# Kernel optimization log

Measured on AMD Instinct MI355X. Metric: run time of the kernel, lower is better.

## Reference

```python
import jax, jax.numpy as jnp
import numpy as np

B, T_D, T_P = 64, 256, 1024
DRUG_DIM, PROT_DIM, D = 128, 128, 128
MAX_LEN = 1024
NEG = -1e9


def _linear_params(k, out_d, in_d):
    k1, k2 = jax.random.split(k)
    lim = 1.0 / np.sqrt(in_d)
    W = jax.random.uniform(k1, (out_d, in_d), minval=-lim, maxval=lim, dtype=jnp.float32)
    b = jax.random.uniform(k2, (out_d,), minval=-lim, maxval=lim, dtype=jnp.float32)
    return W, b


def setup_inputs() -> dict:
    key = jax.random.key(0)
    ks = jax.random.split(key, 13)
    inp = {
        'smiles_embeddings': jax.random.normal(ks[0], (B, T_D, DRUG_DIM), dtype=jnp.float32),
        'protein_embeddings': jax.random.normal(ks[1], (B, T_P, PROT_DIM), dtype=jnp.float32),
        'smiles_mask': jax.random.randint(ks[2], (B, T_D), 0, 2, dtype=jnp.int32),
        'protein_mask': jax.random.randint(ks[3], (B, T_P), 0, 2, dtype=jnp.int32),
        # torch inits pos_bias to zeros; small random values make the test nontrivial
        'pos_bias': 0.02 * jax.random.normal(ks[4], (MAX_LEN, MAX_LEN), dtype=jnp.float32),
    }
    names = [('Wqd', 'bqd', DRUG_DIM), ('Wkp', 'bkp', PROT_DIM), ('Wvp', 'bvp', PROT_DIM),
             ('Wqp', 'bqp', PROT_DIM), ('Wkd', 'bkd', DRUG_DIM), ('Wvd', 'bvd', DRUG_DIM),
             ('Wpd', 'bpd', D), ('Wpp', 'bpp', D)]
    for i, (wn, bn, in_d) in enumerate(names):
        W, b = _linear_params(ks[5 + i], D, in_d)
        inp[wn] = W
        inp[bn] = b
    return inp


def _lin(x, W, b):
    return x @ W.T + b


def _aft(q, k, v, pb_masked, Wp, bp):
    # q: [B,Ti,D]; k,v: [B,Tj,D]; pb_masked: [B,Ti,Tj]
    max_k = k.max(axis=1, keepdims=True)              # per (b,d) over seq j
    max_pb = pb_masked.max(axis=2, keepdims=True)     # per (b,i) over j
    exp_k = jnp.exp(k - max_k)                        # [B,Tj,D]
    exp_pb = jnp.exp(pb_masked - max_pb)              # [B,Ti,Tj]
    num = jnp.einsum('bij,bjd->bid', exp_pb, exp_k * v)
    den = jnp.einsum('bij,bjd->bid', exp_pb, exp_k)
    y = jax.nn.sigmoid(q) * num / den
    return _lin(y, Wp, bp)


def reference(smiles_embeddings, protein_embeddings, smiles_mask, protein_mask, pos_bias,
              Wqd, bqd, Wkp, bkp, Wvp, bvp, Wqp, bqp, Wkd, bkd, Wvd, bvd, Wpd, bpd, Wpp, bpp):
    Td = smiles_embeddings.shape[1]
    Tp = protein_embeddings.shape[1]
    combined = smiles_mask[:, :, None] * protein_mask[:, None, :]  # [B,Td,Tp]
    pb = pos_bias[:Td, :Tp][None]                                   # [1,Td,Tp]

    # drug queries attend over protein keys/values
    pb_d = jnp.where(combined == 0, NEG, pb)
    y_d = _aft(_lin(smiles_embeddings, Wqd, bqd),
               _lin(protein_embeddings, Wkp, bkp),
               _lin(protein_embeddings, Wvp, bvp), pb_d, Wpd, bpd)

    # protein queries attend over drug keys/values (transposed pos bias)
    pb_p = jnp.where(jnp.swapaxes(combined, 1, 2) == 0, NEG, jnp.swapaxes(pb, 1, 2))
    y_p = _aft(_lin(protein_embeddings, Wqp, bqp),
               _lin(smiles_embeddings, Wkd, bkd),
               _lin(smiles_embeddings, Wvd, bvd), pb_p, Wpp, bpp)

    y_d = jnp.where(smiles_mask[:, :, None] == 0, NEG, y_d).max(axis=1)   # [B,D]
    y_p = jnp.where(protein_mask[:, :, None] == 0, NEG, y_p).max(axis=1)  # [B,D]
    return y_d, y_p
```

## Files before the change

### kernel.cpp

```cpp
#include <hip/hip_runtime.h>
#include <cstdint>
#include <cstddef>

#define NEGV -1e9f

typedef __bf16 bf16x8 __attribute__((ext_vector_type(8)));
typedef float f32x4 __attribute__((ext_vector_type(4)));
typedef unsigned short us4 __attribute__((ext_vector_type(4)));
typedef unsigned short us8 __attribute__((ext_vector_type(8)));

__device__ __forceinline__ unsigned short f2bf(float f) {
  unsigned int u = __float_as_uint(f);
  u += 0x7fffu + ((u >> 16) & 1u);
  return (unsigned short)(u >> 16);
}
__device__ __forceinline__ float bf2f(unsigned short u) {
  return __uint_as_float(((unsigned)u) << 16);
}


__global__ void prep_kernel(const float* __restrict__ w0, const float* __restrict__ w1,
                            const float* __restrict__ w2, const float* __restrict__ w3,
                            const float* __restrict__ w4, const float* __restrict__ w5,
                            const float* __restrict__ w6, const float* __restrict__ w7,
                            unsigned short* __restrict__ Wbf,
                            const float* __restrict__ pb,
                            unsigned short* __restrict__ epb,
                            unsigned short* __restrict__ epbT,
                            unsigned int* __restrict__ outEnc) {
  __shared__ unsigned short t[32][33];
  const int blk = blockIdx.x, tid = threadIdx.x;
  if (blk < 64) {
    outEnc[blk * 256 + tid] = 0u;
    return;
  }
  if (blk < 192) {
    const float* Ws[8] = {w0, w1, w2, w3, w4, w5, w6, w7};
    int idx = (blk - 64) * 256 + tid;
    int mat = idx >> 12, off = idx & 4095;
    float4 v = *(const float4*)&Ws[mat][(size_t)off * 4];
    us4 p;
    p.x = f2bf(v.x); p.y = f2bf(v.y); p.z = f2bf(v.z); p.w = f2bf(v.w);
    *(us4*)&Wbf[(size_t)mat * 16384 + (size_t)off * 4] = p;
    return;
  }
  const int bid = blk - 192;
  const int j0 = (bid & 31) * 32, i0 = (bid >> 5) * 32;
  const int tx = tid & 31, ty = tid >> 5;
#pragma unroll
  for (int r = 0; r < 4; ++r) {
    int i = i0 + ty + r * 8;
    unsigned short u = f2bf(__expf(pb[(size_t)i * 1024 + j0 + tx]));
    epb[(size_t)i * 1024 + j0 + tx] = u;
    t[ty + r * 8][tx] = u;
  }
  __syncthreads();
#pragma unroll
  for (int r = 0; r < 4; ++r)
    epbT[(size_t)(j0 + ty + r * 8) * 256 + i0 + tx] = t[tx][ty + r * 8];
}

__global__ __launch_bounds__(256) void proj3_all(
    const float* __restrict__ smiles, const float* __restrict__ prot,
    const int* __restrict__ smask, const int* __restrict__ pmask,
    const unsigned short* __restrict__ Wbf,
    const float* __restrict__ bqd, const float* __restrict__ bkd, const float* __restrict__ bvd,
    const float* __restrict__ bqp, const float* __restrict__ bkp, const float* __restrict__ bvp,
    const unsigned short* __restrict__ epb, const unsigned short* __restrict__ epbT,
    unsigned short* __restrict__ AFd, unsigned short* __restrict__ AFp,
    unsigned short* __restrict__ SQd, unsigned short* __restrict__ BKd,
    unsigned short* __restrict__ BVd,
    unsigned short* __restrict__ SQp, unsigned short* __restrict__ BKp,
    unsigned short* __restrict__ BVp) {
  const int tid = threadIdx.x;

  if (blockIdx.x >= 1280) {
    int sid = (blockIdx.x - 1280) * 256 + tid;
    if (sid < 32768) {
      int lane = sid & 63, kt = (sid >> 6) & 31, it = sid >> 11;
      int i = it * 16 + (lane & 15), j = kt * 32 + (lane >> 4) * 8;
      *(us8*)&AFd[(size_t)sid * 8] = *(const us8*)&epb[(size_t)i * 1024 + j];
    } else {
      int s2 = sid - 32768;
      int lane = s2 & 63, kt = (s2 >> 6) & 7, it = s2 >> 9;
      int i = it * 16 + (lane & 15), j = kt * 32 + (lane >> 4) * 8;
      *(us8*)&AFp[(size_t)s2 * 8] = *(const us8*)&epbT[(size_t)i * 256 + j];
    }
    return;
  }

  __shared__ unsigned short xL[64 * 136];

  const float* X; const int* mask;
  const unsigned short *Wq, *Wk, *Wv;
  const float *bq, *bk_, *bv;
  unsigned short *SQ, *BK, *BV;
  int T, g0;
  if (blockIdx.x < 256) {
    X = smiles; mask = smask; T = 256; g0 = blockIdx.x * 64;
    Wq = Wbf; Wk = Wbf + 16384; Wv = Wbf + 32768;
    bq = bqd; bk_ = bkd; bv = bvd;
    SQ = SQd; BK = BKd; BV = BVd;
  } else {
    X = prot; mask = pmask; T = 1024; g0 = (blockIdx.x - 256) * 64;
    Wq = Wbf + 3 * 16384; Wk = Wbf + 4 * 16384; Wv = Wbf + 5 * 16384;
    bq = bqp; bk_ = bkp; bv = bvp;
    SQ = SQp; BK = BKp; BV = BVp;
  }
  const int b = g0 / T;
  const int tl0 = g0 - b * T;
  const int NIT = T / 16, NKT = T / 32;

#pragma unroll
  for (int r = 0; r < 8; ++r) {
    int i4 = tid + 256 * r;
    int t = i4 >> 5, k4 = (i4 & 31) * 4;
    float4 v = *(const float4*)&X[(size_t)(g0 + t) * 128 + k4];
    us4 p;
    p.x = f2bf(v.x); p.y = f2bf(v.y); p.z = f2bf(v.z); p.w = f2bf(v.w);
    *(us4*)&xL[t * 136 + k4] = p;
  }
  __syncthreads();

  const int lane = tid & 63, wave = tid >> 6;
  const int lo = lane & 15, hi = lane >> 4;
  const int d0 = wave * 32;

  f32x4 aQ[4][2], aK[4][2], aV[4][2];
#pragma unroll
  for (int a = 0; a < 4; ++a)
#pragma unroll
    for (int s = 0; s < 2; ++s)
#pragma unroll
      for (int r = 0; r < 4; ++r) { aQ[a][s][r] = 0.f; aK[a][s][r] = 0.f; aV[a][s][r] = 0.f; }

#pragma unroll
  for (int kt = 0; kt < 128; kt += 32) {
    bf16x8 bQ[2], bK[2], bV[2];
#pragma unroll
    for (int s = 0; s < 2; ++s) {
      size_t roff = (size_t)(d0 + s * 16 + lo) * 128 + kt + hi * 8;
      bQ[s] = *(const bf16x8*)&Wq[roff];
      bK[s] = *(const bf16x8*)&Wk[roff];
      bV[s] = *(const bf16x8*)&Wv[roff];
    }
#pragma unroll
    for (int a = 0; a < 4; ++a) {
      bf16x8 af = *(const bf16x8*)&xL[(a * 16 + lo) * 136 + kt + hi * 8];
#pragma unroll
      for (int s = 0; s < 2; ++s) {
        aQ[a][s] = __builtin_amdgcn_mfma_f32_16x16x32_bf16(af, bQ[s], aQ[a][s], 0, 0, 0);
        aK[a][s] = __builtin_amdgcn_mfma_f32_16x16x32_bf16(af, bK[s], aK[a][s], 0, 0, 0);
        aV[a][s] = __builtin_amdgcn_mfma_f32_16x16x32_bf16(af, bV[s], aV[a][s], 0, 0, 0);
      }
    }
  }

#pragma unroll
  for (int s = 0; s < 2; ++s) {
    int dt = (d0 >> 4) + s;
    float bb = bq[d0 + s * 16 + lo];
#pragma unroll
    for (int a = 0; a < 4; ++a) {
      int it = (tl0 >> 4) + a;
      us4 v;
#pragma unroll
      for (int r = 0; r < 4; ++r) {
        float q = aQ[a][s][r] + bb;
        v[r] = f2bf(1.f / (1.f + __expf(-q)));
      }
      ((us4*)SQ)[(((size_t)b * NIT + it) * 8 + dt) * 64 + lane] = v;
    }
  }

#pragma unroll
  for (int s = 0; s < 2; ++s) {
    int dt = (d0 >> 4) + s;
    float bbk = bk_[d0 + s * 16 + lo], bbv = bv[d0 + s * 16 + lo];
#pragma unroll
    for (int a = 0; a < 4; ++a) {
      int kt = (tl0 >> 5) + (a >> 1);
      int lane_f = ((a & 1) * 2 + (hi >> 1)) * 16 + lo;
      us4 vk, vv;
#pragma unroll
      for (int r = 0; r < 4; ++r) {
        int tg = g0 + a * 16 + hi * 4 + r;
        int mk = mask[tg];
        float ek = mk ? __expf(aK[a][s][r] + bbk) : 0.f;
        float ekv = ek * (aV[a][s][r] + bbv);
        vk[r] = f2bf(ek);
        vv[r] = f2bf(ekv);
      }
      size_t q4 = ((((size_t)b * NKT + kt) * 8 + dt) * 64 + lane_f) * 2 + (hi & 1);
      ((us4*)BK)[q4] = vk;
      ((us4*)BV)[q4] = vv;
    }
  }
}

__global__ __launch_bounds__(256, 3) void aft_all(
    const unsigned short* __restrict__ AFd, const unsigned short* __restrict__ AFp,
    const unsigned short* __restrict__ SQd, const unsigned short* __restrict__ BKd,
    const unsigned short* __restrict__ BVd,
    const unsigned short* __restrict__ SQp, const unsigned short* __restrict__ BKp,
    const unsigned short* __restrict__ BVp,
    const int* __restrict__ smask, const int* __restrict__ pmask,
    const unsigned short* __restrict__ Wbf,
    const float* __restrict__ bpd, const float* __restrict__ bpp,
    unsigned int* __restrict__ outEnc) {
  __shared__ unsigned short smem[8192 + 64 * 136];
  unsigned short* denL = smem;
  unsigned short* yL = smem + 8192;

  const int blk = blockIdx.x;
  const unsigned short *AF, *BK, *BV, *SQ, *Wp;
  const float* bp;
  const int* msk;
  unsigned int* oEnc;
  int b, i0, NKT, NIT;
  if (blk < 256) {
    b = blk & 63; i0 = (blk >> 6) * 64; NKT = 32; NIT = 16;
    AF = AFd; BK = BKp; BV = BVp; SQ = SQd;
    Wp = Wbf + 6 * 16384; bp = bpd; msk = smask + b * 256 + i0; oEnc = outEnc;
  } else {
    int k = blk - 256;
    b = k & 63; i0 = (k >> 6) * 64; NKT = 8; NIT = 64;
    AF = AFp; BK = BKd; BV = BVd; SQ = SQp;
    Wp = Wbf + 7 * 16384; bp = bpp; msk = pmask + b * 1024 + i0; oEnc = outEnc + 8192;
  }

  const int tid = threadIdx.x, lane = tid & 63, w = tid >> 6;
  const int lo = lane & 15, hi = lane >> 4;
  const int h = w & 1;
  const int isden = w >> 1;
  const int it0 = i0 >> 4;
  const int dt0 = h * 4;

  const unsigned short* Bb = (isden ? BK : BV) + (size_t)b * NKT * 8 * 64 * 8;

  f32x4 acc[4][4];
#pragma unroll
  for (int a = 0; a < 4; ++a)
#pragma unroll
    for (int n = 0; n < 4; ++n)
#pragma unroll
      for (int r = 0; r < 4; ++r) acc[a][n][r] = 0.f;

  bf16x8 af[4], bb[4];
#pragma unroll
  for (int a = 0; a < 4; ++a)
    af[a] = *(const bf16x8*)&AF[(((size_t)(it0 + a) * NKT + 0) * 64 + lane) * 8];
#pragma unroll
  for (int n = 0; n < 4; ++n)
    bb[n] = *(const bf16x8*)&Bb[(((size_t)0 * 8 + dt0 + n) * 64 + lane) * 8];

  for (int kt = 0; kt < NKT; ++kt) {
    const int k2 = (kt + 1 < NKT) ? kt + 1 : kt;
    bf16x8 afn[4], bbn[4];
#pragma unroll
    for (int a = 0; a < 4; ++a)
      afn[a] = *(const bf16x8*)&AF[(((size_t)(it0 + a) * NKT + k2) * 64 + lane) * 8];
#pragma unroll
    for (int n = 0; n < 4; ++n)
      bbn[n] = *(const bf16x8*)&Bb[(((size_t)k2 * 8 + dt0 + n) * 64 + lane) * 8];
#pragma unroll
    for (int a = 0; a < 4; ++a)
#pragma unroll
      for (int n = 0; n < 4; ++n)
        acc[a][n] = __builtin_amdgcn_mfma_f32_16x16x32_bf16(af[a], bb[n], acc[a][n], 0, 0, 0);
#pragma unroll
    for (int a = 0; a < 4; ++a) af[a] = afn[a];
#pragma unroll
    for (int n = 0; n < 4; ++n) bb[n] = bbn[n];
  }

  if (isden) {
#pragma unroll
    for (int a = 0; a < 4; ++a)
#pragma unroll
      for (int n = 0; n < 4; ++n) {
        us4 v;
#pragma unroll
        for (int r = 0; r < 4; ++r) v[r] = f2bf(acc[a][n][r]);
        ((us4*)denL)[((h * 4 + a) * 4 + n) * 64 + lane] = v;
      }
  }
  __syncthreads();

  if (!isden) {
#pragma unroll
    for (int a = 0; a < 4; ++a)
#pragma unroll
      for (int n = 0; n < 4; ++n) {
        us4 dv = ((const us4*)denL)[((h * 4 + a) * 4 + n) * 64 + lane];
        us4 q = ((const us4*)SQ)[(((size_t)b * NIT + it0 + a) * 8 + dt0 + n) * 64 + lane];
        int iL = a * 16 + hi * 4;
        int d = h * 64 + n * 16 + lo;
#pragma unroll
        for (int r = 0; r < 4; ++r) {
          float y = bf2f(q[r]) * __fdividef(acc[a][n][r], bf2f(dv[r]));
          yL[(iL + r) * 136 + d] = f2bf(y);
        }
      }
  }
  __syncthreads();

  const int wi2 = w * 16;
  f32x4 aZ[8];
#pragma unroll
  for (int n = 0; n < 8; ++n)
#pragma unroll
    for (int r = 0; r < 4; ++r) aZ[n][r] = 0.f;

#pragma unroll
  for (int kt = 0; kt < 128; kt += 32) {
    bf16x8 af2 = *(const bf16x8*)&yL[(wi2 + lo) * 136 + kt + hi * 8];
#pragma unroll
    for (int n = 0; n < 8; ++n) {
      bf16x8 bw = *(const bf16x8*)&Wp[(size_t)(n * 16 + lo) * 128 + kt + hi * 8];
      aZ[n] = __builtin_amdgcn_mfma_f32_16x16x32_bf16(af2, bw, aZ[n], 0, 0, 0);
    }
  }

#pragma unroll
  for (int n = 0; n < 8; ++n) {
    int d = n * 16 + lo;
    float bbia = bp[d];
    float m = NEGV;
#pragma unroll
    for (int r = 0; r < 4; ++r) {
      int iL = wi2 + hi * 4 + r;
      float z = aZ[n][r] + bbia;
      m = msk[iL] ? fmaxf(m, z) : m;
    }
    m = fmaxf(m, __shfl_xor(m, 16, 64));
    m = fmaxf(m, __shfl_xor(m, 32, 64));
    if (hi == 0) {
      unsigned bits = __float_as_uint(m);
      unsigned key = (bits & 0x80000000u) ? ~bits : (bits | 0x80000000u);
      atomicMax(&oEnc[b * 128 + d], key);
    }
  }
}

__global__ void out_decode(unsigned int* o) {
  int i = blockIdx.x * 256 + threadIdx.x;
  unsigned k = o[i];
  unsigned bits = (k & 0x80000000u) ? (k ^ 0x80000000u) : ~k;
  ((float*)o)[i] = __uint_as_float(bits);
}

extern "C" void kernel_launch(void* const* d_in, const int* in_sizes, int n_in,
                              void* d_out, int out_size, void* d_ws, size_t ws_size,
                              hipStream_t stream) {
  const float* smiles = (const float*)d_in[0];
  const float* prot   = (const float*)d_in[1];
  const int* smask = (const int*)d_in[2];
  const int* pmask = (const int*)d_in[3];
  const float* pos_bias = (const float*)d_in[4];
  const float* Wqd = (const float*)d_in[5];  const float* bqd = (const float*)d_in[6];
  const float* Wkp = (const float*)d_in[7];  const float* bkp = (const float*)d_in[8];
  const float* Wvp = (const float*)d_in[9];  const float* bvp = (const float*)d_in[10];
  const float* Wqp = (const float*)d_in[11]; const float* bqp = (const float*)d_in[12];
  const float* Wkd = (const float*)d_in[13]; const float* bkd = (const float*)d_in[14];
  const float* Wvd = (const float*)d_in[15]; const float* bvd = (const float*)d_in[16];
  const float* Wpd = (const float*)d_in[17]; const float* bpd = (const float*)d_in[18];
  const float* Wpp = (const float*)d_in[19]; const float* bpp = (const float*)d_in[20];

  unsigned short* u = (unsigned short*)d_ws;
  unsigned short* BKp_  = u;
  unsigned short* BVp_  = BKp_ + 8388608;
  unsigned short* BKd_  = BVp_ + 8388608;
  unsigned short* BVd_  = BKd_ + 2097152;
  unsigned short* SQd_  = BVd_ + 2097152;
  unsigned short* SQp_  = SQd_ + 2097152;
  unsigned short* epb_  = SQp_ + 8388608;
  unsigned short* epbT_ = epb_ + 262144;
  unsigned short* AFd_  = epbT_ + 262144;
  unsigned short* AFp_  = AFd_ + 262144;
  unsigned short* Wbf   = AFp_ + 262144;

  prep_kernel<<<448, 256, 0, stream>>>(Wqd, Wkd, Wvd, Wqp, Wkp, Wvp, Wpd, Wpp,
                                       Wbf, pos_bias, epb_, epbT_,
                                       (unsigned int*)d_out);

  proj3_all<<<1536, 256, 0, stream>>>(smiles, prot, smask, pmask, Wbf,
                                      bqd, bkd, bvd, bqp, bkp, bvp,
                                      epb_, epbT_, AFd_, AFp_,
                                      SQd_, BKd_, BVd_, SQp_, BKp_, BVp_);

  aft_all<<<1280, 256, 0, stream>>>(AFd_, AFp_, SQd_, BKd_, BVd_,
                                    SQp_, BKp_, BVp_, smask, pmask, Wbf,
                                    bpd, bpp, (unsigned int*)d_out);

  out_decode<<<64, 256, 0, stream>>>((unsigned int*)d_out);
}
```

Baseline: 190.5 us.

## Stage AFT GEMM operands in LDS via direct global-to-LDS loads with larger tiles

The AFT kernel goes from 256-thread blocks covering 64 query rows to 512-thread blocks covering 128 rows. Each k-step, the operand tiles for the exp-bias matrix and the exp(k)·v and exp(k) values are loaded cooperatively into shared memory with global_load_lds. Waves then read them from LDS, so each tile is fetched from global memory once and shared by several waves instead of being loaded per wave into registers. In exchange, the register double-buffered prefetch is gone and there are two block barriers per k-step, which may expose load latency. The tail of the kernel (the projection stage past the shown code) is not visible, so it is unclear whether it was adapted to 128 rows and 8 waves.

```diff
diff --git a/kernel.cpp b/kernel.cpp
--- a/kernel.cpp
+++ b/kernel.cpp
@@ -16,6 +16,12 @@
 }
 __device__ __forceinline__ float bf2f(unsigned short u) {
   return __uint_as_float(((unsigned)u) << 16);
+}
+
+__device__ __forceinline__ void gld16(const void* g, void* l) {
+  __builtin_amdgcn_global_load_lds(
+      (const __attribute__((address_space(1))) unsigned int*)g,
+      (__attribute__((address_space(3))) unsigned int*)l, 16, 0, 0);
 }
 
 
@@ -198,7 +204,7 @@
   }
 }
 
-__global__ __launch_bounds__(256, 3) void aft_all(
+__global__ __launch_bounds__(512, 4) void aft_all(
     const unsigned short* __restrict__ AFd, const unsigned short* __restrict__ AFp,
     const unsigned short* __restrict__ SQd, const unsigned short* __restrict__ BKd,
     const unsigned short* __restrict__ BVd,
@@ -208,9 +214,9 @@
     const unsigned short* __restrict__ Wbf,
     const float* __restrict__ bpd, const float* __restrict__ bpp,
     unsigned int* __restrict__ outEnc) {
-  __shared__ unsigned short smem[8192 + 64 * 136];
-  unsigned short* denL = smem;
-  unsigned short* yL = smem + 8192;
+  __shared__ unsigned short smem[16384 + 128 * 136];
+  unsigned short* sL = smem;
+  unsigned short* yL = smem + 16384;
 
   const int blk = blockIdx.x;
   const unsigned short *AF, *BK, *BV, *SQ, *Wp;
@@ -218,25 +224,26 @@
   const int* msk;
   unsigned int* oEnc;
   int b, i0, NKT, NIT;
-  if (blk < 256) {
-    b = blk & 63; i0 = (blk >> 6) * 64; NKT = 32; NIT = 16;
+  if (blk < 128) {
+    b = blk & 63; i0 = (blk >> 6) * 128; NKT = 32; NIT = 16;
     AF = AFd; BK = BKp; BV = BVp; SQ = SQd;
     Wp = Wbf + 6 * 16384; bp = bpd; msk = smask + b * 256 + i0; oEnc = outEnc;
   } else {
-    int k = blk - 256;
-    b = k & 63; i0 = (k >> 6) * 64; NKT = 8; NIT = 64;
+    int k = blk - 128;
+    b = k & 63; i0 = (k >> 6) * 128; NKT = 8; NIT = 64;
     AF = AFp; BK = BKd; BV = BVd; SQ = SQp;
     Wp = Wbf + 7 * 16384; bp = bpp; msk = pmask + b * 1024 + i0; oEnc = outEnc + 8192;
   }
 
   const int tid = threadIdx.x, lane = tid & 63, w = tid >> 6;
   const int lo = lane & 15, hi = lane >> 4;
-  const int h = w & 1;
-  const int isden = w >> 1;
-  const int it0 = i0 >> 4;
-  const int dt0 = h * 4;
-
-  const unsigned short* Bb = (isden ? BK : BV) + (size_t)b * NKT * 8 * 64 * 8;
+  const int role = w >> 2;
+  const int ih = (w >> 1) & 1, dh = w & 1;
+  const int itg0 = i0 >> 4;
+  const int dt0 = dh * 4;
+
+  const unsigned short* BVb = BV + (size_t)b * NKT * 8 * 512;
+  const unsigned short* BKb = BK + (size_t)b * NKT * 8 * 512;
 
   f32x4 acc[4][4];
 #pragma unroll
@@ -246,35 +253,34 @@
 #pragma unroll
       for (int r = 0; r < 4; ++r) acc[a][n][r] = 0.f;
 
-  bf16x8 af[4], bb[4];
-#pragma unroll
-  for (int a = 0; a < 4; ++a)
-    af[a] = *(const bf16x8*)&AF[(((size_t)(it0 + a) * NKT + 0) * 64 + lane) * 8];
-#pragma unroll
-  for (int n = 0; n < 4; ++n)
-    bb[n] = *(const bf16x8*)&Bb[(((size_t)0 * 8 + dt0 + n) * 64 + lane) * 8];
-
   for (int kt = 0; kt < NKT; ++kt) {
-    const int k2 = (kt + 1 < NKT) ? kt + 1 : kt;
-    bf16x8 afn[4], bbn[4];
+    __syncthreads();
+#pragma unroll
+    for (int j = 0; j < 3; ++j) {
+      int c = w * 3 + j;
+      const unsigned short* src;
+      if (c < 8)       src = AF + (size_t)((itg0 + c) * NKT + kt) * 512;
+      else if (c < 16) src = BVb + (size_t)(kt * 8 + (c - 8)) * 512;
+      else             src = BKb + (size_t)(kt * 8 + (c - 16)) * 512;
+      gld16(src + lane * 8, sL + c * 512);
+    }
+    __syncthreads();
+    bf16x8 af[4], bb[4];
 #pragma unroll
     for (int a = 0; a < 4; ++a)
-      afn[a] = *(const bf16x8*)&AF[(((size_t)(it0 + a) * NKT + k2) * 64 + lane) * 8];
+      af[a] = *(const bf16x8*)&sL[(ih * 4 + a) * 512 + lane * 8];
 #pragma unroll
     for (int n = 0; n < 4; ++n)
-      bbn[n] = *(const bf16x8*)&Bb[(((size_t)k2 * 8 + dt0 + n) * 64 + lane) * 8];
+      bb[n] = *(const bf16x8*)&sL[(8 + role * 8 + dt0 + n) * 512 + lane * 8];
 #pragma unroll
     for (int a = 0; a < 4; ++a)
 #pragma unroll
       for (int n = 0; n < 4; ++n)
         acc[a][n] = __builtin_amdgcn_mfma_f32_16x16x32_bf16(af[a], bb[n], acc[a][n], 0, 0, 0);
-#pragma unroll
-    for (int a = 0; a < 4; ++a) af[a] = afn[a];
-#pragma unroll
-    for (int n = 0; n < 4; ++n) bb[n] = bbn[n];
-  }
-
-  if (isden) {
+  }
+
+  __syncthreads();
+  if (role == 1) {
 #pragma unroll
     for (int a = 0; a < 4; ++a)
 #pragma unroll
@@ -282,20 +288,20 @@
         us4 v;
 #pragma unroll
         for (int r = 0; r < 4; ++r) v[r] = f2bf(acc[a][n][r]);
-        ((us4*)denL)[((h * 4 + a) * 4 + n) * 64 + lane] = v;
+        ((us4*)sL)[((((ih * 2 + dh) * 4 + a) * 4 + n)) * 64 + lane] = v;
       }
   }
   __syncthreads();
 
-  if (!isden) {
+  if (role == 0) {
 #pragma unroll
     for (int a = 0; a < 4; ++a)
 #pragma unroll
       for (int n = 0; n < 4; ++n) {
-        us4 dv = ((const us4*)denL)[((h * 4 + a) * 4 + n) * 64 + lane];
-        us4 q = ((const us4*)SQ)[(((size_t)b * NIT + it0 + a) * 8 + dt0 + n) * 64 + lane];
-        int iL = a * 16 + hi * 4;
-        int d = h * 64 + n * 16 + lo;
+        us4 dv = ((const us4*)sL)[((((ih * 2 + dh) * 4 + a) * 4 + n)) * 64 + lane];
+        us4 q = ((const us4*)SQ)[(((size_t)b * NIT + itg0 + ih * 4 + a) * 8 + dt0 + n) * 64 + lane];
+        int iL = ih * 64 + a * 16 + hi * 4;
+        int d = dh * 64 + n * 16 + lo;
 #pragma unroll
         for (int r = 0; r < 4; ++r) {
           float y = bf2f(q[r]) * __fdividef(acc[a][n][r], bf2f(dv[r]));
@@ -389,9 +395,9 @@
                                       epb_, epbT_, AFd_, AFp_,
                                       SQd_, BKd_, BVd_, SQp_, BKp_, BVp_);
 
-  aft_all<<<1280, 256, 0, stream>>>(AFd_, AFp_, SQd_, BKd_, BVd_,
-                                    SQp_, BKp_, BVp_, smask, pmask, Wbf,
-                                    bpd, bpp, (unsigned int*)d_out);
+  aft_all<<<640, 512, 0, stream>>>(AFd_, AFp_, SQd_, BKd_, BVd_,
+                                   SQp_, BKp_, BVp_, smask, pmask, Wbf,
+                                   bpd, bpp, (unsigned int*)d_out);
 
   out_decode<<<64, 256, 0, stream>>>((unsigned int*)d_out);
 }
```

Measured after the change: 199.9 us. 5.0% more time.
